# Kernel tuning notes

Hardware: AMD Instinct MI355X
Metric: run time of the kernel (lower is better)

Reference implementation:

```python
import jax, jax.numpy as jnp
import numpy as np

B, CIN, H, W = 8, 1, 512, 512
KS = 3            # kernel size
KK = KS * KS      # 9 sampling points
COUT = 3
HO, WO = H - 2, W - 2  # stride=1, pad=0, dil=1


def setup_inputs() -> dict:
    key = jax.random.key(0)
    k1, k2, k3, k4, k5 = jax.random.split(key, 5)
    x = jax.random.normal(k1, (B, CIN, H, W), jnp.float32)
    offset = jax.random.normal(k2, (B, 2 * KK, HO, WO), jnp.float32)
    mask = jax.random.uniform(k3, (B, KK, HO, WO), jnp.float32)
    # kaiming-ish scale for a 3x3 conv with fan_in = CIN*9
    weight = jax.random.normal(k4, (COUT, CIN, KS, KS), jnp.float32) / 3.0
    bias = jax.random.normal(k5, (COUT,), jnp.float32) * 0.1
    return {"x": x, "offset": offset, "mask": mask, "weight": weight, "bias": bias}


def _bilinear_sample(img, py, px):
    # img: [C,H,W]; py/px: [KK,HO,WO] fractional sample coords (zero padding)
    Himg, Wimg = img.shape[1], img.shape[2]
    y0 = jnp.floor(py)
    x0 = jnp.floor(px)
    ly = py - y0  # bilinear weights
    lx = px - x0

    def corner(yc, xc):
        yi = jnp.clip(yc, 0, Himg - 1).astype(jnp.int32)
        xi = jnp.clip(xc, 0, Wimg - 1).astype(jnp.int32)
        valid = ((yc >= 0) & (yc <= Himg - 1) & (xc >= 0) & (xc <= Wimg - 1))
        # gather -> [C,KK,HO,WO], zero out-of-bounds corners
        return img[:, yi, xi] * valid.astype(img.dtype)[None]

    v00 = corner(y0, x0)
    v01 = corner(y0, x0 + 1.0)
    v10 = corner(y0 + 1.0, x0)
    v11 = corner(y0 + 1.0, x0 + 1.0)
    return (v00 * (1 - ly) * (1 - lx) + v01 * (1 - ly) * lx
            + v10 * ly * (1 - lx) + v11 * ly * lx)  # [C,KK,HO,WO]


def _deform_conv2d(x, offset, mask, weight, bias):
    Bn, C = x.shape[0], x.shape[1]
    off = offset.reshape(Bn, KK, 2, HO, WO)  # [:, :, 0]=dy, [:, :, 1]=dx (torchvision layout)
    kh = (jnp.arange(KK) // KS).astype(jnp.float32)  # kernel row per sampling point
    kw = (jnp.arange(KK) % KS).astype(jnp.float32)
    # base grid (stride=1, pad=0, dil=1) + kernel tap + learned offset -> [B,KK,HO,WO]
    py = off[:, :, 0] + jnp.arange(HO, dtype=jnp.float32)[None, None, :, None] + kh[None, :, None, None]
    px = off[:, :, 1] + jnp.arange(WO, dtype=jnp.float32)[None, None, None, :] + kw[None, :, None, None]
    sampled = jax.vmap(_bilinear_sample)(x, py, px)        # [B,C,KK,HO,WO]
    sampled = sampled * mask[:, None]                       # modulation mask
    w = weight.reshape(weight.shape[0], C, KK)
    out = jnp.einsum('ock,bckhw->bohw', w, sampled)
    return out + bias[None, :, None, None]


def reference(x, offset, mask, weight, bias):
    return _deform_conv2d(x, offset, mask, weight, bias)
```

## Files before the change

kernel.cpp:

```cpp
#include <hip/hip_runtime.h>

#define B_    8
#define H_    512
#define W_    512
#define KK_   9
#define COUT_ 3
#define HO_   510
#define WO_   510
#define PLANE_ 260100

__device__ __forceinline__ int iclamp(int v, int lo, int hi) {
    return v < lo ? lo : (v > hi ? hi : v);
}

typedef float f2  __attribute__((ext_vector_type(2)));
typedef float f2a __attribute__((ext_vector_type(2), aligned(4)));

__global__ __launch_bounds__(512, 4) void dcn_fwd_kernel(
    const float* __restrict__ x,
    const float* __restrict__ offset,
    const float* __restrict__ mask,
    const float* __restrict__ weight,
    const float* __restrict__ bias,
    float* __restrict__ out)
{
    const int bid  = blockIdx.x;
    const int wt   = bid & 1;
    const int band = (bid >> 1) & 127;
    const int b    = bid >> 8;

    const int tid  = threadIdx.x;
    const int wave = tid >> 6;
    const int lane = tid & 63;
    const int r    = lane >> 4;
    const int c    = lane & 15;

    int ho = band * 4 + r;
    const bool vrow = (ho < HO_);
    if (!vrow) ho = HO_ - 1;
    int wo0 = wt * 256 + wave * 32 + 2 * c;
    if (wo0 > WO_ - 2) wo0 = WO_ - 2;

    const int pix = ho * WO_ + wo0;
    const float* xb   = x + (b << 18);
    const float* offb = offset + b * (2 * KK_ * PLANE_) + pix;
    const float* mb   = mask   + b * (KK_ * PLANE_)    + pix;

    float w0[KK_], w1[KK_], w2[KK_];
    #pragma unroll
    for (int k = 0; k < KK_; ++k) {
        w0[k] = weight[0 * KK_ + k];
        w1[k] = weight[1 * KK_ + k];
        w2[k] = weight[2 * KK_ + k];
    }
    const float b0 = bias[0], b1 = bias[1], b2 = bias[2];

    const float fho = (float)ho;
    const float fwo = (float)wo0;

    float a00 = 0.f, a01 = 0.f;
    float a10 = 0.f, a11 = 0.f;
    float a20 = 0.f, a21 = 0.f;

    #pragma unroll
    for (int kh = 0; kh < 3; ++kh) {
        #pragma unroll
        for (int kw = 0; kw < 3; ++kw) {
            const int kk = kh * 3 + kw;
            const f2 dy2 = *(const f2*)(offb + (2 * kk)     * PLANE_);
            const f2 dx2 = *(const f2*)(offb + (2 * kk + 1) * PLANE_);
            const f2 m2  = *(const f2*)(mb   +  kk          * PLANE_);

            #pragma unroll
            for (int p = 0; p < 2; ++p) {
                const float py = (fho + (float)kh) + dy2[p];
                const float px = (fwo + (float)(kw + p)) + dx2[p];

                const float y0f = floorf(py);
                const float x0f = floorf(px);
                const float ly  = py - y0f;
                const float lx  = px - x0f;
                const float y1f = y0f + 1.0f;
                const float x1f = x0f + 1.0f;

                const float vy0 = (y0f >= 0.f && y0f <= 511.f) ? 1.f : 0.f;
                const float vy1 = (y1f >= 0.f && y1f <= 511.f) ? 1.f : 0.f;
                const float vx0 = (x0f >= 0.f && x0f <= 511.f) ? 1.f : 0.f;
                const float vx1 = (x1f >= 0.f && x1f <= 511.f) ? 1.f : 0.f;

                const int iy0 = (int)y0f;
                const int ix0 = (int)x0f;
                const int yi0 = iclamp(iy0,     0, 511);
                const int yi1 = iclamp(iy0 + 1, 0, 511);
                const int xc0 = iclamp(ix0,     0, 510);

                const f2a q0 = *(const f2a*)(xb + (yi0 << 9) + xc0);
                const f2a q1 = *(const f2a*)(xb + (yi1 << 9) + xc0);

                const bool hi = (x0f >= 511.f);
                const bool lo = (x0f < 0.f);

                const float v00 = (hi ? q0.y : q0.x) * (vy0 * vx0);
                const float v01 = (lo ? q0.x : q0.y) * (vy0 * vx1);
                const float v10 = (hi ? q1.y : q1.x) * (vy1 * vx0);
                const float v11 = (lo ? q1.x : q1.y) * (vy1 * vx1);

                const float top = fmaf(lx, v01 - v00, v00);
                const float bot = fmaf(lx, v11 - v10, v10);
                const float val = fmaf(ly, bot - top, top);
                const float s   = val * m2[p];

                if (p == 0) {
                    a00 = fmaf(w0[kk], s, a00);
                    a10 = fmaf(w1[kk], s, a10);
                    a20 = fmaf(w2[kk], s, a20);
                } else {
                    a01 = fmaf(w0[kk], s, a01);
                    a11 = fmaf(w1[kk], s, a11);
                    a21 = fmaf(w2[kk], s, a21);
                }
            }
        }
    }

    if (vrow) {
        const int ob = b * (COUT_ * PLANE_) + pix;
        f2 o0 = {a00 + b0, a01 + b0};
        f2 o1 = {a10 + b1, a11 + b1};
        f2 o2 = {a20 + b2, a21 + b2};
        *(f2*)(out + ob)              = o0;
        *(f2*)(out + ob + PLANE_)     = o1;
        *(f2*)(out + ob + 2 * PLANE_) = o2;
    }
}

extern "C" void kernel_launch(void* const* d_in, const int* in_sizes, int n_in,
                              void* d_out, int out_size, void* d_ws, size_t ws_size,
                              hipStream_t stream) {
    const float* x      = (const float*)d_in[0];
    const float* offset = (const float*)d_in[1];
    const float* mask   = (const float*)d_in[2];
    const float* weight = (const float*)d_in[3];
    const float* bias   = (const float*)d_in[4];
    float* out = (float*)d_out;

    const int grid = 2 * 128 * B_;
    dcn_fwd_kernel<<<grid, 512, 0, stream>>>(x, offset, mask, weight, bias, out);
}
```

Baseline: 64.23 us.

## Stage input halo tile in LDS for bilinear gathers with global fallback

Each block cooperatively loads a 22x276 halo tile of the input image into shared memory. Bilinear corner reads come from LDS when the sample falls in the tile, with a bounds-checked global fallback otherwise. Threads are remapped so each block row is covered by 128 threads. This aims to cut the scattered global gather traffic, at the cost of a prologue load, a barrier and LDS usage that may limit occupancy.

```diff
diff --git a/kernel.cpp b/kernel.cpp
--- a/kernel.cpp
+++ b/kernel.cpp
@@ -9,12 +9,16 @@
 #define WO_   510
 #define PLANE_ 260100
 
+#define TR_    4
+#define XROWS_ 22
+#define XCOLS_ 276
+#define NCHK_  69
+
+typedef float f2 __attribute__((ext_vector_type(2)));
+
 __device__ __forceinline__ int iclamp(int v, int lo, int hi) {
     return v < lo ? lo : (v > hi ? hi : v);
 }
-
-typedef float f2  __attribute__((ext_vector_type(2)));
-typedef float f2a __attribute__((ext_vector_type(2), aligned(4)));
 
 __global__ __launch_bounds__(512, 4) void dcn_fwd_kernel(
     const float* __restrict__ x,
@@ -24,25 +28,42 @@
     const float* __restrict__ bias,
     float* __restrict__ out)
 {
+    __shared__ float sx[XROWS_ * XCOLS_];
+
     const int bid  = blockIdx.x;
     const int wt   = bid & 1;
     const int band = (bid >> 1) & 127;
     const int b    = bid >> 8;
 
-    const int tid  = threadIdx.x;
-    const int wave = tid >> 6;
-    const int lane = tid & 63;
-    const int r    = lane >> 4;
-    const int c    = lane & 15;
+    const int ho0 = band * TR_;
+    const int cb  = wt * 256;
+    const int XR0 = ho0 - 8;
+    const int XC0 = cb - 8;
 
-    int ho = band * 4 + r;
+    const float* xb = x + (b << 18);
+
+    for (int i = threadIdx.x; i < XROWS_ * NCHK_; i += 512) {
+        const int wr  = i / NCHK_;
+        const int ck  = i - wr * NCHK_;
+        const int yr  = XR0 + wr;
+        const int col = XC0 + 4 * ck;
+        float4 v = make_float4(0.f, 0.f, 0.f, 0.f);
+        if (((unsigned)yr < 512u) & ((unsigned)col <= 508u))
+            v = *(const float4*)(xb + (yr << 9) + col);
+        *(float4*)(&sx[wr * XCOLS_ + 4 * ck]) = v;
+    }
+    __syncthreads();
+
+    const int tid = threadIdx.x;
+    const int r   = tid >> 7;
+    const int c   = tid & 127;
+    int ho = ho0 + r;
     const bool vrow = (ho < HO_);
     if (!vrow) ho = HO_ - 1;
-    int wo0 = wt * 256 + wave * 32 + 2 * c;
+    int wo0 = cb + 2 * c;
     if (wo0 > WO_ - 2) wo0 = WO_ - 2;
 
     const int pix = ho * WO_ + wo0;
-    const float* xb   = x + (b << 18);
     const float* offb = offset + b * (2 * KK_ * PLANE_) + pix;
     const float* mb   = mask   + b * (KK_ * PLANE_)    + pix;
 
@@ -80,30 +101,33 @@
                 const float x0f = floorf(px);
                 const float ly  = py - y0f;
                 const float lx  = px - x0f;
-                const float y1f = y0f + 1.0f;
-                const float x1f = x0f + 1.0f;
 
-                const float vy0 = (y0f >= 0.f && y0f <= 511.f) ? 1.f : 0.f;
-                const float vy1 = (y1f >= 0.f && y1f <= 511.f) ? 1.f : 0.f;
-                const float vx0 = (x0f >= 0.f && x0f <= 511.f) ? 1.f : 0.f;
-                const float vx1 = (x1f >= 0.f && x1f <= 511.f) ? 1.f : 0.f;
+                const int iy = (int)y0f - XR0;
+                const int ix = (int)x0f - XC0;
 
-                const int iy0 = (int)y0f;
-                const int ix0 = (int)x0f;
-                const int yi0 = iclamp(iy0,     0, 511);
-                const int yi1 = iclamp(iy0 + 1, 0, 511);
-                const int xc0 = iclamp(ix0,     0, 510);
-
-                const f2a q0 = *(const f2a*)(xb + (yi0 << 9) + xc0);
-                const f2a q1 = *(const f2a*)(xb + (yi1 << 9) + xc0);
-
-                const bool hi = (x0f >= 511.f);
-                const bool lo = (x0f < 0.f);
-
-                const float v00 = (hi ? q0.y : q0.x) * (vy0 * vx0);
-                const float v01 = (lo ? q0.x : q0.y) * (vy0 * vx1);
-                const float v10 = (hi ? q1.y : q1.x) * (vy1 * vx0);
-                const float v11 = (lo ? q1.x : q1.y) * (vy1 * vx1);
+                float v00, v01, v10, v11;
+                if (__builtin_expect(((unsigned)iy <= (unsigned)(XROWS_ - 2)) &
+                                     ((unsigned)ix <= (unsigned)(XCOLS_ - 2)), 1)) {
+                    const int a = iy * XCOLS_ + ix;
+                    v00 = sx[a];
+                    v01 = sx[a + 1];
+                    v10 = sx[a + XCOLS_];
+                    v11 = sx[a + XCOLS_ + 1];
+                } else {
+                    const float y1f = y0f + 1.0f, x1f = x0f + 1.0f;
+                    const float vy0 = (y0f >= 0.f && y0f <= 511.f) ? 1.f : 0.f;
+                    const float vy1 = (y1f >= 0.f && y1f <= 511.f) ? 1.f : 0.f;
+                    const float vx0 = (x0f >= 0.f && x0f <= 511.f) ? 1.f : 0.f;
+                    const float vx1 = (x1f >= 0.f && x1f <= 511.f) ? 1.f : 0.f;
+                    const int yi0 = iclamp((int)y0f, 0, 511);
+                    const int yi1 = iclamp((int)y0f + 1, 0, 511);
+                    const int xi0 = iclamp((int)x0f, 0, 511);
+                    const int xi1 = iclamp((int)x0f + 1, 0, 511);
+                    v00 = xb[(yi0 << 9) + xi0] * (vy0 * vx0);
+                    v01 = xb[(yi0 << 9) + xi1] * (vy0 * vx1);
+                    v10 = xb[(yi1 << 9) + xi0] * (vy1 * vx0);
+                    v11 = xb[(yi1 << 9) + xi1] * (vy1 * vx1);
+                }
 
                 const float top = fmaf(lx, v01 - v00, v00);
                 const float bot = fmaf(lx, v11 - v10, v10);
```

Result: slower. 197.0 us (+206.8%).
